# Performance work log

Measured on AMD Instinct MI355X. Metric: run time of the kernel, lower is better.

Reference implementation:

```python
import jax, jax.numpy as jnp
import numpy as np

# MXFP4 e2m1 value lookup (sign bit is the high bit of the nibble)
FP4_LUT = jnp.array([0.0, 0.5, 1.0, 1.5, 2.0, 3.0, 4.0, 6.0,
                     -0.0, -0.5, -1.0, -1.5, -2.0, -3.0, -4.0, -6.0], dtype=jnp.float32)
BLOCK = 32  # mxfp4 scale block size
TOP_K = 2


def dequant_mxfp4(blocks, scales):
    # blocks: [..., K//2] packed uint8 nibbles (low nibble = even elem, high = odd)
    # scales: [..., K//BLOCK] e8m0 biased exponents; scale = 2**(s - 127)
    b = blocks.astype(jnp.int32)
    lo = b & 0xF
    hi = (b >> 4) & 0xF
    nib = jnp.stack([lo, hi], axis=-1).reshape(blocks.shape[:-1] + (blocks.shape[-1] * 2,))
    vals = FP4_LUT[nib]                                   # [..., K]
    s = jnp.exp2(scales.astype(jnp.float32) - 127.0)      # [..., K//BLOCK]
    s = jnp.repeat(s, BLOCK, axis=-1)                     # [..., K]
    return vals * s


def setup_inputs() -> dict:
    key = jax.random.key(0)
    ks = jax.random.split(key, 8)
    E, H, F, B, S = 16, 1024, 2048, 1, 128
    hidden_states = jax.random.normal(ks[0], (B, S, H), dtype=jnp.float32)
    router_w = jax.random.normal(ks[1], (E, H), dtype=jnp.float32) * 0.05
    blocks_gu = jax.random.randint(ks[2], (E, 2 * F, H // 2), 0, 256, dtype=jnp.int32)
    scales_gu = jax.random.randint(ks[3], (E, 2 * F, H // BLOCK), 118, 130, dtype=jnp.int32)
    bias_gu = jax.random.normal(ks[4], (E, 2 * F), dtype=jnp.float32) * 0.02
    blocks_down = jax.random.randint(ks[5], (E, H, F // 2), 0, 256, dtype=jnp.int32)
    scales_down = jax.random.randint(ks[6], (E, H, F // BLOCK), 118, 130, dtype=jnp.int32)
    bias_down = jax.random.normal(ks[7], (E, H), dtype=jnp.float32) * 0.02
    return {"hidden_states": hidden_states, "router_w": router_w,
            "bias_gu": bias_gu, "bias_down": bias_down,
            "blocks_gu": blocks_gu, "scales_gu": scales_gu,
            "blocks_down": blocks_down, "scales_down": scales_down}


def reference(hidden_states, router_w, bias_gu, bias_down,
              blocks_gu, scales_gu, blocks_down, scales_down):
    B, S, H = hidden_states.shape
    flat = hidden_states.reshape(-1, H)                   # [T, H]
    T = flat.shape[0]
    E = router_w.shape[0]

    # --- routing: topk_then_softmax (default softmax_order) ---
    logits = flat @ router_w.T                            # [T, E]
    top_vals, top_idx = jax.lax.top_k(logits, TOP_K)      # [T, K]
    weights = jax.nn.softmax(top_vals, axis=-1).astype(flat.dtype)
    combine = jnp.zeros((T, E), flat.dtype).at[jnp.arange(T)[:, None], top_idx].set(weights)

    # --- mxfp4 dequant of fused expert weights ---
    w_gu = dequant_mxfp4(blocks_gu, scales_gu)            # [E, 2F, H]
    w_down = dequant_mxfp4(blocks_down, scales_down)      # [E, H, F]

    # --- expert MLP (SwiGLU), combined with routing weights ---
    gu = jnp.einsum('th,eoh->eto', flat, w_gu) + bias_gu[:, None, :]   # [E, T, 2F]
    gate, up = jnp.split(gu, 2, axis=-1)
    h = jax.nn.silu(gate) * up                            # [E, T, F]
    y = jnp.einsum('etf,ehf->eth', h, w_down) + bias_down[:, None, :]  # [E, T, H]
    out = jnp.einsum('eth,te->th', y, combine)            # [T, H]
    return out.reshape(B, S, H)
```

## Files before the change

kernel.cpp:

```cpp
#include <hip/hip_runtime.h>
#include <hip/hip_fp16.h>
#include <math.h>

#define NE 16
#define HD 1024
#define FD 2048

typedef _Float16 half8 __attribute__((ext_vector_type(8)));
typedef float f32x4 __attribute__((ext_vector_type(4)));

#define TOPI_OFF 0
#define TOPW_OFF 256
#define CNT_OFF  512
#define PREF_OFF 528
#define SLOT_OFF 544
#define INVT_OFF 800
#define META_OFF 1056
#define TL1_OFF  1060
#define HBUF_OFF 4096
#define Y0_OFF   (HBUF_OFF + 262144)
#define Y1_OFF   (Y0_OFF + 262144)

union XI { int4 v; half8 h; };

__device__ __forceinline__ int fp4h(int nib) {
    int c = nib & 7;
    int v;
    if (c == 0) v = 0;
    else if (c == 1) v = 14 << 10;
    else v = (((c >> 1) + 14) << 10) | ((c & 1) << 9);
    v |= (nib & 8) << 12;
    return v;
}

__device__ __forceinline__ int dec2i(const int* lut, int byte, int sv) {
    int l = lut[byte & 255];
    __half2 p = *reinterpret_cast<const __half2*>(&l);
    __half2 sc = *reinterpret_cast<const __half2*>(&sv);
    __half2 r = __hmul2(p, sc);
    return *reinterpret_cast<int*>(&r);
}

__global__ void routing_kernel(const float* __restrict__ x, const float* __restrict__ rw,
                               int* __restrict__ top_idx, float* __restrict__ top_w) {
    int t = blockIdx.x;
    int tid = threadIdx.x;
    int e = tid >> 4, seg = tid & 15;
    const float* xr = x + t * HD + seg * 64;
    const float* wr = rw + e * HD + seg * 64;
    float p = 0.f;
    #pragma unroll 8
    for (int i = 0; i < 64; ++i) p += xr[i] * wr[i];
    __shared__ float part[16][16];
    __shared__ float logit[16];
    part[e][seg] = p;
    __syncthreads();
    if (tid < 16) {
        float s = 0.f;
        #pragma unroll
        for (int i = 0; i < 16; ++i) s += part[tid][i];
        logit[tid] = s;
    }
    __syncthreads();
    if (tid == 0) {
        int i0 = 0; float v0 = logit[0];
        #pragma unroll
        for (int i = 1; i < 16; ++i) { if (logit[i] > v0) { v0 = logit[i]; i0 = i; } }
        int i1 = -1; float v1 = -1e30f;
        #pragma unroll
        for (int i = 0; i < 16; ++i) { if (i != i0 && logit[i] > v1) { v1 = logit[i]; i1 = i; } }
        float w0 = 1.f / (1.f + expf(v1 - v0));
        float w1 = 1.f / (1.f + expf(v0 - v1));
        top_idx[t * 2]     = i0;  top_w[t * 2]     = w0;
        top_idx[t * 2 + 1] = i1;  top_w[t * 2 + 1] = w1;
    }
}

__global__ void build_kernel(const int* __restrict__ top_idx,
                             int* __restrict__ cnt, int* __restrict__ pref,
                             int* __restrict__ slot, int* __restrict__ invtok,
                             int* __restrict__ meta, int* __restrict__ tl1) {
    __shared__ int scnt[16], spref[16], scur[16];
    int tid = threadIdx.x;
    if (tid < 16) scnt[tid] = 0;
    __syncthreads();
    int e = top_idx[tid];
    atomicAdd(&scnt[e], 1);
    __syncthreads();
    if (tid == 0) {
        int s = 0;
        for (int i = 0; i < 16; ++i) { spref[i] = s; pref[i] = s; cnt[i] = scnt[i]; s += scnt[i]; }
        int m1 = 0;
        for (int i = 0; i < 16; ++i) {
            int ntile1 = (scnt[i] + 15) >> 4;
            for (int m = 0; m < ntile1; ++m) tl1[m1++] = (i << 8) | m;
        }
        meta[0] = m1;
    }
    if (tid < 16) scur[tid] = 0;
    __syncthreads();
    int pos = spref[e] + atomicAdd(&scur[e], 1);
    slot[tid] = pos;
    invtok[pos] = tid >> 1;
}

__global__ __launch_bounds__(256) void gemm1_mfma(
    const float* __restrict__ x, const int* __restrict__ invtok,
    const int* __restrict__ qblk, const int* __restrict__ qscl,
    const float* __restrict__ bias,
    const int* __restrict__ cnt, const int* __restrict__ pref,
    const int* __restrict__ meta, const int* __restrict__ tl1,
    _Float16* __restrict__ hbuf) {
    __shared__ int lut[256];
    __shared__ int4 Asb[2][128];
    __shared__ int4 Bsb[2][512];
    __shared__ float exch[4][64][4];
    int tid = threadIdx.x;
    lut[tid] = fp4h(tid & 15) | (fp4h(tid >> 4) << 16);
    int wave = tid >> 6, lane = tid & 63;
    int bl = lane & 15, kb4 = lane >> 4;
    int rloc = wave * 16 + bl;
    int rs = tid >> 2, kq = tid & 3;
    int tok = tid >> 4, jj = tid & 15;
    int a2idx = (tok * 8 + ((jj >> 1) ^ (tok & 7))) * 2 + (jj & 1);
    int nwork = meta[0] << 6;

    for (int w = blockIdx.x; w < nwork; w += gridDim.x) {
        int tile = tl1[w >> 6];
        int fc = w & 63;
        int e = tile >> 8, mt = tile & 255;
        int n = cnt[e];
        int nt = n - mt * 16; if (nt > 16) nt = 16;
        int base = pref[e];
        int t0 = base + mt * 16;
        int f0 = fc * 32;

        long rowg = (long)e * 4096 + ((rs < 32) ? (f0 + rs) : (2048 + f0 + rs - 32));
        const int4* wrow = (const int4*)(qblk + rowg * 512);
        const int* srow = qscl + rowg * 32;
        int gtok = invtok[t0 + ((tok < nt) ? tok : nt - 1)];
        const int4* arow = (const int4*)x + (long)gtok * 256;

        int4 q0 = wrow[kq * 2];
        int4 q1 = wrow[kq * 2 + 1];
        int sc = srow[kq >> 1];
        int4 av = arow[jj];
        __syncthreads();
        {
            union { int4 v; float f[4]; } uf; uf.v = av;
            union { _Float16 h[4]; int2 p; } o;
            o.h[0] = (_Float16)uf.f[0]; o.h[1] = (_Float16)uf.f[1];
            o.h[2] = (_Float16)uf.f[2]; o.h[3] = (_Float16)uf.f[3];
            ((int2*)Asb[0])[a2idx] = o.p;
            int sv = (sc - 112) << 10; sv |= sv << 16;
            int4 o0, o1;
            o0.x = dec2i(lut, q0.x, sv); o0.y = dec2i(lut, q0.y, sv);
            o0.z = dec2i(lut, q0.z, sv); o0.w = dec2i(lut, q0.w, sv);
            o1.x = dec2i(lut, q1.x, sv); o1.y = dec2i(lut, q1.y, sv);
            o1.z = dec2i(lut, q1.z, sv); o1.w = dec2i(lut, q1.w, sv);
            Bsb[0][rs * 8 + ((kq * 2) ^ (rs & 7))] = o0;
            Bsb[0][rs * 8 + ((kq * 2 + 1) ^ (rs & 7))] = o1;
        }
        __syncthreads();

        f32x4 acc = {0.f, 0.f, 0.f, 0.f};
        for (int kb = 0; kb < 16; ++kb) {
            int cur = kb & 1;
            if (kb < 15) {
                q0 = wrow[(kb + 1) * 8 + kq * 2];
                q1 = wrow[(kb + 1) * 8 + kq * 2 + 1];
                sc = srow[(kb + 1) * 2 + (kq >> 1)];
                av = arow[(kb + 1) * 16 + jj];
            }
            #pragma unroll
            for (int ks = 0; ks < 2; ++ks) {
                int g = ks * 4 + kb4;
                XI a, b;
                a.v = Asb[cur][bl * 8 + (g ^ (bl & 7))];
                b.v = Bsb[cur][rloc * 8 + (g ^ (rloc & 7))];
                acc = __builtin_amdgcn_mfma_f32_16x16x32_f16(a.h, b.h, acc, 0, 0, 0);
            }
            if (kb < 15) {
                int nxt = cur ^ 1;
                union { int4 v; float f[4]; } uf; uf.v = av;
                union { _Float16 h[4]; int2 p; } o;
                o.h[0] = (_Float16)uf.f[0]; o.h[1] = (_Float16)uf.f[1];
                o.h[2] = (_Float16)uf.f[2]; o.h[3] = (_Float16)uf.f[3];
                ((int2*)Asb[nxt])[a2idx] = o.p;
                int sv = (sc - 112) << 10; sv |= sv << 16;
                int4 o0, o1;
                o0.x = dec2i(lut, q0.x, sv); o0.y = dec2i(lut, q0.y, sv);
                o0.z = dec2i(lut, q0.z, sv); o0.w = dec2i(lut, q0.w, sv);
                o1.x = dec2i(lut, q1.x, sv); o1.y = dec2i(lut, q1.y, sv);
                o1.z = dec2i(lut, q1.z, sv); o1.w = dec2i(lut, q1.w, sv);
                Bsb[nxt][rs * 8 + ((kq * 2) ^ (rs & 7))] = o0;
                Bsb[nxt][rs * 8 + ((kq * 2 + 1) ^ (rs & 7))] = o1;
                __syncthreads();
            }
        }
        #pragma unroll
        for (int i = 0; i < 4; ++i) exch[wave][lane][i] = acc[i];
        __syncthreads();
        int fl = tid & 31, wv = fl >> 4, col = fl & 15;
        float bg = bias[(long)e * 4096 + f0 + fl];
        float bu = bias[(long)e * 4096 + 2048 + f0 + fl];
        #pragma unroll
        for (int d = 0; d < 2; ++d) {
            int tk = (tid >> 5) + d * 8;
            int ln = ((tk >> 2) << 4) | col;
            int rg = tk & 3;
            float g = exch[wv][ln][rg] + bg;
            float u = exch[wv + 2][ln][rg] + bu;
            float h = (g / (1.f + expf(-g))) * u;
            if (tk < nt)
                hbuf[(long)(t0 + tk) * FD + f0 + fl] = (_Float16)(h * 0.0625f);
        }
        __syncthreads();
    }
}

__global__ __launch_bounds__(256) void gemm2_mfma(
    const _Float16* __restrict__ hbuf, const int* __restrict__ qblk,
    const int* __restrict__ qscl, const float* __restrict__ bias,
    const int* __restrict__ cnt, const int* __restrict__ pref,
    const int* __restrict__ meta, const int* __restrict__ tl1,
    float* __restrict__ y0p, float* __restrict__ y1p) {
    __shared__ int lut[256];
    __shared__ int4 Asb[2][128];
    __shared__ int4 Bsb[2][512];
    int tid = threadIdx.x;
    lut[tid] = fp4h(tid & 15) | (fp4h(tid >> 4) << 16);
    int wave = tid >> 6, lane = tid & 63;
    int bl = lane & 15, kb4 = lane >> 4;
    int rloc = wave * 16 + bl;
    int rs = tid >> 2, kq = tid & 3;
    int tok = tid >> 3, ga = tid & 7;
    int nwork = meta[0] << 5;

    for (int w = blockIdx.x; w < nwork; w += gridDim.x) {
        int tile = tl1[w >> 5];
        int sub = w & 31;
        int hc = sub & 15, kh = sub >> 4;
        int e = tile >> 8, mt = tile & 255;
        int n = cnt[e];
        int nt = n - mt * 16; if (nt > 16) nt = 16;
        int base = pref[e];
        int t0 = base + mt * 16;
        int h0 = hc * 64;

        long rowg = (long)e * HD + h0 + rs;
        const int4* wrow = (const int4*)(qblk + rowg * 1024) + (kh * 16) * 8;
        const int* srow = qscl + rowg * 64 + kh * 32;
        int tclamp = (tok < nt) ? tok : nt - 1;
        const int4* arow = (const int4*)hbuf + (long)(t0 + tclamp) * 256 + (kh * 16) * 8;

        int4 q0 = wrow[kq * 2];
        int4 q1 = wrow[kq * 2 + 1];
        int sc = srow[kq >> 1];
        int4 av;
        if (tid < 128) av = arow[ga];
        __syncthreads();
        if (tid < 128) Asb[0][tok * 8 + (ga ^ (tok & 7))] = av;
        {
            int sv = (sc - 112) << 10; sv |= sv << 16;
            int4 o0, o1;
            o0.x = dec2i(lut, q0.x, sv); o0.y = dec2i(lut, q0.y, sv);
            o0.z = dec2i(lut, q0.z, sv); o0.w = dec2i(lut, q0.w, sv);
            o1.x = dec2i(lut, q1.x, sv); o1.y = dec2i(lut, q1.y, sv);
            o1.z = dec2i(lut, q1.z, sv); o1.w = dec2i(lut, q1.w, sv);
            Bsb[0][rs * 8 + ((kq * 2) ^ (rs & 7))] = o0;
            Bsb[0][rs * 8 + ((kq * 2 + 1) ^ (rs & 7))] = o1;
        }
        __syncthreads();

        f32x4 acc = {0.f, 0.f, 0.f, 0.f};
        for (int kb = 0; kb < 16; ++kb) {
            int cur = kb & 1;
            if (kb < 15) {
                q0 = wrow[(kb + 1) * 8 + kq * 2];
                q1 = wrow[(kb + 1) * 8 + kq * 2 + 1];
                sc = srow[(kb + 1) * 2 + (kq >> 1)];
                if (tid < 128) av = arow[(kb + 1) * 8 + ga];
            }
            #pragma unroll
            for (int ks = 0; ks < 2; ++ks) {
                int g = ks * 4 + kb4;
                XI a, b;
                a.v = Asb[cur][bl * 8 + (g ^ (bl & 7))];
                b.v = Bsb[cur][rloc * 8 + (g ^ (rloc & 7))];
                acc = __builtin_amdgcn_mfma_f32_16x16x32_f16(a.h, b.h, acc, 0, 0, 0);
            }
            if (kb < 15) {
                int nxt = cur ^ 1;
                if (tid < 128) Asb[nxt][tok * 8 + (ga ^ (tok & 7))] = av;
                int sv = (sc - 112) << 10; sv |= sv << 16;
                int4 o0, o1;
                o0.x = dec2i(lut, q0.x, sv); o0.y = dec2i(lut, q0.y, sv);
                o0.z = dec2i(lut, q0.z, sv); o0.w = dec2i(lut, q0.w, sv);
                o1.x = dec2i(lut, q1.x, sv); o1.y = dec2i(lut, q1.y, sv);
                o1.z = dec2i(lut, q1.z, sv); o1.w = dec2i(lut, q1.w, sv);
                Bsb[nxt][rs * 8 + ((kq * 2) ^ (rs & 7))] = o0;
                Bsb[nxt][rs * 8 + ((kq * 2 + 1) ^ (rs & 7))] = o1;
                __syncthreads();
            }
        }
        int hcol = h0 + wave * 16 + bl;
        float bv = (kh == 0) ? bias[(long)e * HD + hcol] : 0.f;
        float* yp = (kh == 0) ? y0p : y1p;
        #pragma unroll
        for (int r = 0; r < 4; ++r) {
            int row = kb4 * 4 + r;
            if (row < nt)
                yp[(long)(t0 + row) * HD + hcol] = acc[r] * 16.f + bv;
        }
        __syncthreads();
    }
}

__global__ void combine_kernel(const float* __restrict__ y0, const float* __restrict__ y1,
                               const int* __restrict__ slot, const float* __restrict__ topw,
                               float* __restrict__ out) {
    int t = blockIdx.x;
    int i = threadIdx.x;
    int s0 = slot[2 * t], s1 = slot[2 * t + 1];
    float w0 = topw[2 * t], w1 = topw[2 * t + 1];
    float4 a0 = ((const float4*)(y0 + (long)s0 * HD))[i];
    float4 a1 = ((const float4*)(y1 + (long)s0 * HD))[i];
    float4 b0 = ((const float4*)(y0 + (long)s1 * HD))[i];
    float4 b1 = ((const float4*)(y1 + (long)s1 * HD))[i];
    float4 o;
    o.x = w0 * (a0.x + a1.x) + w1 * (b0.x + b1.x);
    o.y = w0 * (a0.y + a1.y) + w1 * (b0.y + b1.y);
    o.z = w0 * (a0.z + a1.z) + w1 * (b0.z + b1.z);
    o.w = w0 * (a0.w + a1.w) + w1 * (b0.w + b1.w);
    ((float4*)(out + (long)t * HD))[i] = o;
}

extern "C" void kernel_launch(void* const* d_in, const int* in_sizes, int n_in,
                              void* d_out, int out_size, void* d_ws, size_t ws_size,
                              hipStream_t stream) {
    const float* x          = (const float*)d_in[0];
    const float* rw         = (const float*)d_in[1];
    const float* bias_gu    = (const float*)d_in[2];
    const float* bias_down  = (const float*)d_in[3];
    const int*   blocks_gu  = (const int*)d_in[4];
    const int*   scales_gu  = (const int*)d_in[5];
    const int*   blocks_down= (const int*)d_in[6];
    const int*   scales_down= (const int*)d_in[7];
    float* out = (float*)d_out;
    int*   wsI = (int*)d_ws;
    float* wsF = (float*)d_ws;
    _Float16* hbuf = (_Float16*)(wsI + HBUF_OFF);
    float*    y0   = wsF + Y0_OFF;
    float*    y1   = wsF + Y1_OFF;

    routing_kernel<<<128, 256, 0, stream>>>(x, rw, wsI + TOPI_OFF, wsF + TOPW_OFF);
    build_kernel<<<1, 256, 0, stream>>>(wsI + TOPI_OFF, wsI + CNT_OFF, wsI + PREF_OFF,
                                        wsI + SLOT_OFF, wsI + INVT_OFF,
                                        wsI + META_OFF, wsI + TL1_OFF);
    gemm1_mfma<<<2048, 256, 0, stream>>>(x, wsI + INVT_OFF, blocks_gu, scales_gu, bias_gu,
                                         wsI + CNT_OFF, wsI + PREF_OFF,
                                         wsI + META_OFF, wsI + TL1_OFF, hbuf);
    gemm2_mfma<<<1024, 256, 0, stream>>>(hbuf, blocks_down, scales_down, bias_down,
                                         wsI + CNT_OFF, wsI + PREF_OFF,
                                         wsI + META_OFF, wsI + TL1_OFF, y0, y1);
    combine_kernel<<<128, 256, 0, stream>>>(y0, y1, wsI + SLOT_OFF, wsF + TOPW_OFF, out);
}
```

Before: 60.74 us.

## Deepen global-load prefetch to two stages and use LDS-only barriers in expert GEMMs

Both expert GEMM kernels now keep two K-blocks of weights and activations in flight in registers, and the K loop is fully unrolled in pairs with fixed LDS buffers. The plain __syncthreads is replaced by an inline-asm barrier that waits only on LDS counters, so outstanding global loads are not drained at each barrier. The goal is to hide global memory latency behind dequant and MFMA work, at the cost of more registers and a hand-written barrier that depends on correct waitcnt semantics. The routing dot product is also vectorised to float4 loads with fma.

```diff
diff --git a/kernel.cpp b/kernel.cpp
--- a/kernel.cpp
+++ b/kernel.cpp
@@ -23,6 +23,8 @@
 
 union XI { int4 v; half8 h; };
 
+#define BARRIER_LDS() asm volatile("s_waitcnt lgkmcnt(0)\ns_barrier" ::: "memory")
+
 __device__ __forceinline__ int fp4h(int nib) {
     int c = nib & 7;
     int v;
@@ -41,16 +43,39 @@
     return *reinterpret_cast<int*>(&r);
 }
 
+__device__ __forceinline__ void stageB(const int* lut, int4* Bbuf, int rs, int kq,
+                                       int4 q0, int4 q1, int sc) {
+    int sv = (sc - 112) << 10; sv |= sv << 16;
+    int4 o0, o1;
+    o0.x = dec2i(lut, q0.x, sv); o0.y = dec2i(lut, q0.y, sv);
+    o0.z = dec2i(lut, q0.z, sv); o0.w = dec2i(lut, q0.w, sv);
+    o1.x = dec2i(lut, q1.x, sv); o1.y = dec2i(lut, q1.y, sv);
+    o1.z = dec2i(lut, q1.z, sv); o1.w = dec2i(lut, q1.w, sv);
+    Bbuf[rs * 8 + ((kq * 2) ^ (rs & 7))] = o0;
+    Bbuf[rs * 8 + ((kq * 2 + 1) ^ (rs & 7))] = o1;
+}
+
+__device__ __forceinline__ void stageA1(int4* Abuf, int a2idx, int4 av) {
+    union { int4 v; float f[4]; } uf; uf.v = av;
+    union { _Float16 h[4]; int2 p; } o;
+    o.h[0] = (_Float16)uf.f[0]; o.h[1] = (_Float16)uf.f[1];
+    o.h[2] = (_Float16)uf.f[2]; o.h[3] = (_Float16)uf.f[3];
+    ((int2*)Abuf)[a2idx] = o.p;
+}
+
 __global__ void routing_kernel(const float* __restrict__ x, const float* __restrict__ rw,
                                int* __restrict__ top_idx, float* __restrict__ top_w) {
     int t = blockIdx.x;
     int tid = threadIdx.x;
     int e = tid >> 4, seg = tid & 15;
-    const float* xr = x + t * HD + seg * 64;
-    const float* wr = rw + e * HD + seg * 64;
+    const float4* xr = (const float4*)(x + t * HD + seg * 64);
+    const float4* wr = (const float4*)(rw + e * HD + seg * 64);
     float p = 0.f;
-    #pragma unroll 8
-    for (int i = 0; i < 64; ++i) p += xr[i] * wr[i];
+    #pragma unroll
+    for (int i = 0; i < 16; ++i) {
+        float4 a = xr[i], b = wr[i];
+        p = fmaf(a.x, b.x, fmaf(a.y, b.y, fmaf(a.z, b.z, fmaf(a.w, b.w, p))));
+    }
     __shared__ float part[16][16];
     __shared__ float logit[16];
     part[e][seg] = p;
@@ -141,62 +166,60 @@
         int gtok = invtok[t0 + ((tok < nt) ? tok : nt - 1)];
         const int4* arow = (const int4*)x + (long)gtok * 256;
 
-        int4 q0 = wrow[kq * 2];
-        int4 q1 = wrow[kq * 2 + 1];
-        int sc = srow[kq >> 1];
-        int4 av = arow[jj];
-        __syncthreads();
-        {
-            union { int4 v; float f[4]; } uf; uf.v = av;
-            union { _Float16 h[4]; int2 p; } o;
-            o.h[0] = (_Float16)uf.f[0]; o.h[1] = (_Float16)uf.f[1];
-            o.h[2] = (_Float16)uf.f[2]; o.h[3] = (_Float16)uf.f[3];
-            ((int2*)Asb[0])[a2idx] = o.p;
-            int sv = (sc - 112) << 10; sv |= sv << 16;
-            int4 o0, o1;
-            o0.x = dec2i(lut, q0.x, sv); o0.y = dec2i(lut, q0.y, sv);
-            o0.z = dec2i(lut, q0.z, sv); o0.w = dec2i(lut, q0.w, sv);
-            o1.x = dec2i(lut, q1.x, sv); o1.y = dec2i(lut, q1.y, sv);
-            o1.z = dec2i(lut, q1.z, sv); o1.w = dec2i(lut, q1.w, sv);
-            Bsb[0][rs * 8 + ((kq * 2) ^ (rs & 7))] = o0;
-            Bsb[0][rs * 8 + ((kq * 2 + 1) ^ (rs & 7))] = o1;
-        }
-        __syncthreads();
+        int4 c0q0 = wrow[kq * 2], c0q1 = wrow[kq * 2 + 1];
+        int  c0sc = srow[kq >> 1];
+        int4 c0av = arow[jj];
+        __syncthreads();
+        stageA1(Asb[0], a2idx, c0av);
+        stageB(lut, Bsb[0], rs, kq, c0q0, c0q1, c0sc);
+        int4 aq0 = wrow[8 + kq * 2], aq1 = wrow[8 + kq * 2 + 1];
+        int  asc = srow[2 + (kq >> 1)];
+        int4 aav = arow[16 + jj];
+        int4 bq0 = wrow[16 + kq * 2], bq1 = wrow[16 + kq * 2 + 1];
+        int  bsc = srow[4 + (kq >> 1)];
+        int4 bav = arow[32 + jj];
+        BARRIER_LDS();
 
         f32x4 acc = {0.f, 0.f, 0.f, 0.f};
-        for (int kb = 0; kb < 16; ++kb) {
-            int cur = kb & 1;
-            if (kb < 15) {
-                q0 = wrow[(kb + 1) * 8 + kq * 2];
-                q1 = wrow[(kb + 1) * 8 + kq * 2 + 1];
-                sc = srow[(kb + 1) * 2 + (kq >> 1)];
-                av = arow[(kb + 1) * 16 + jj];
-            }
+        #pragma unroll
+        for (int p = 0; p < 8; ++p) {
+            int kb = 2 * p;
             #pragma unroll
             for (int ks = 0; ks < 2; ++ks) {
                 int g = ks * 4 + kb4;
                 XI a, b;
-                a.v = Asb[cur][bl * 8 + (g ^ (bl & 7))];
-                b.v = Bsb[cur][rloc * 8 + (g ^ (rloc & 7))];
+                a.v = Asb[0][bl * 8 + (g ^ (bl & 7))];
+                b.v = Bsb[0][rloc * 8 + (g ^ (rloc & 7))];
                 acc = __builtin_amdgcn_mfma_f32_16x16x32_f16(a.h, b.h, acc, 0, 0, 0);
             }
-            if (kb < 15) {
-                int nxt = cur ^ 1;
-                union { int4 v; float f[4]; } uf; uf.v = av;
-                union { _Float16 h[4]; int2 p; } o;
-                o.h[0] = (_Float16)uf.f[0]; o.h[1] = (_Float16)uf.f[1];
-                o.h[2] = (_Float16)uf.f[2]; o.h[3] = (_Float16)uf.f[3];
-                ((int2*)Asb[nxt])[a2idx] = o.p;
-                int sv = (sc - 112) << 10; sv |= sv << 16;
-                int4 o0, o1;
-                o0.x = dec2i(lut, q0.x, sv); o0.y = dec2i(lut, q0.y, sv);
-                o0.z = dec2i(lut, q0.z, sv); o0.w = dec2i(lut, q0.w, sv);
-                o1.x = dec2i(lut, q1.x, sv); o1.y = dec2i(lut, q1.y, sv);
-                o1.z = dec2i(lut, q1.z, sv); o1.w = dec2i(lut, q1.w, sv);
-                Bsb[nxt][rs * 8 + ((kq * 2) ^ (rs & 7))] = o0;
-                Bsb[nxt][rs * 8 + ((kq * 2 + 1) ^ (rs & 7))] = o1;
-                __syncthreads();
-            }
+            stageA1(Asb[1], a2idx, aav);
+            stageB(lut, Bsb[1], rs, kq, aq0, aq1, asc);
+            if (p < 7) {
+                int s = kb + 3;
+                aq0 = wrow[s * 8 + kq * 2]; aq1 = wrow[s * 8 + kq * 2 + 1];
+                asc = srow[s * 2 + (kq >> 1)];
+                aav = arow[s * 16 + jj];
+            }
+            BARRIER_LDS();
+            #pragma unroll
+            for (int ks = 0; ks < 2; ++ks) {
+                int g = ks * 4 + kb4;
+                XI a, b;
+                a.v = Asb[1][bl * 8 + (g ^ (bl & 7))];
+                b.v = Bsb[1][rloc * 8 + (g ^ (rloc & 7))];
+                acc = __builtin_amdgcn_mfma_f32_16x16x32_f16(a.h, b.h, acc, 0, 0, 0);
+            }
+            if (p < 7) {
+                stageA1(Asb[0], a2idx, bav);
+                stageB(lut, Bsb[0], rs, kq, bq0, bq1, bsc);
+                if (p < 6) {
+                    int s = kb + 4;
+                    bq0 = wrow[s * 8 + kq * 2]; bq1 = wrow[s * 8 + kq * 2 + 1];
+                    bsc = srow[s * 2 + (kq >> 1)];
+                    bav = arow[s * 16 + jj];
+                }
+            }
+            BARRIER_LDS();
         }
         #pragma unroll
         for (int i = 0; i < 4; ++i) exch[wave][lane][i] = acc[i];
@@ -235,6 +258,7 @@
     int rloc = wave * 16 + bl;
     int rs = tid >> 2, kq = tid & 3;
     int tok = tid >> 3, ga = tid & 7;
+    int aidx = tok * 8 + (ga ^ (tok & 7));
     int nwork = meta[0] << 5;
 
     for (int w = blockIdx.x; w < nwork; w += gridDim.x) {
@@ -254,55 +278,61 @@
         int tclamp = (tok < nt) ? tok : nt - 1;
         const int4* arow = (const int4*)hbuf + (long)(t0 + tclamp) * 256 + (kh * 16) * 8;
 
-        int4 q0 = wrow[kq * 2];
-        int4 q1 = wrow[kq * 2 + 1];
-        int sc = srow[kq >> 1];
-        int4 av;
-        if (tid < 128) av = arow[ga];
-        __syncthreads();
-        if (tid < 128) Asb[0][tok * 8 + (ga ^ (tok & 7))] = av;
-        {
-            int sv = (sc - 112) << 10; sv |= sv << 16;
-            int4 o0, o1;
-            o0.x = dec2i(lut, q0.x, sv); o0.y = dec2i(lut, q0.y, sv);
-            o0.z = dec2i(lut, q0.z, sv); o0.w = dec2i(lut, q0.w, sv);
-            o1.x = dec2i(lut, q1.x, sv); o1.y = dec2i(lut, q1.y, sv);
-            o1.z = dec2i(lut, q1.z, sv); o1.w = dec2i(lut, q1.w, sv);
-            Bsb[0][rs * 8 + ((kq * 2) ^ (rs & 7))] = o0;
-            Bsb[0][rs * 8 + ((kq * 2 + 1) ^ (rs & 7))] = o1;
-        }
-        __syncthreads();
+        int4 c0q0 = wrow[kq * 2], c0q1 = wrow[kq * 2 + 1];
+        int  c0sc = srow[kq >> 1];
+        int4 c0av;
+        if (tid < 128) c0av = arow[ga];
+        __syncthreads();
+        if (tid < 128) Asb[0][aidx] = c0av;
+        stageB(lut, Bsb[0], rs, kq, c0q0, c0q1, c0sc);
+        int4 aq0 = wrow[8 + kq * 2], aq1 = wrow[8 + kq * 2 + 1];
+        int  asc = srow[2 + (kq >> 1)];
+        int4 aav; if (tid < 128) aav = arow[8 + ga];
+        int4 bq0 = wrow[16 + kq * 2], bq1 = wrow[16 + kq * 2 + 1];
+        int  bsc = srow[4 + (kq >> 1)];
+        int4 bav; if (tid < 128) bav = arow[16 + ga];
+        BARRIER_LDS();
 
         f32x4 acc = {0.f, 0.f, 0.f, 0.f};
-        for (int kb = 0; kb < 16; ++kb) {
-            int cur = kb & 1;
-            if (kb < 15) {
-                q0 = wrow[(kb + 1) * 8 + kq * 2];
-                q1 = wrow[(kb + 1) * 8 + kq * 2 + 1];
-                sc = srow[(kb + 1) * 2 + (kq >> 1)];
-                if (tid < 128) av = arow[(kb + 1) * 8 + ga];
-            }
+        #pragma unroll
+        for (int p = 0; p < 8; ++p) {
+            int kb = 2 * p;
             #pragma unroll
             for (int ks = 0; ks < 2; ++ks) {
                 int g = ks * 4 + kb4;
                 XI a, b;
-                a.v = Asb[cur][bl * 8 + (g ^ (bl & 7))];
-                b.v = Bsb[cur][rloc * 8 + (g ^ (rloc & 7))];
+                a.v = Asb[0][bl * 8 + (g ^ (bl & 7))];
+                b.v = Bsb[0][rloc * 8 + (g ^ (rloc & 7))];
                 acc = __builtin_amdgcn_mfma_f32_16x16x32_f16(a.h, b.h, acc, 0, 0, 0);
             }
-            if (kb < 15) {
-                int nxt = cur ^ 1;
-                if (tid < 128) Asb[nxt][tok * 8 + (ga ^ (tok & 7))] = av;
-                int sv = (sc - 112) << 10; sv |= sv << 16;
-                int4 o0, o1;
-                o0.x = dec2i(lut, q0.x, sv); o0.y = dec2i(lut, q0.y, sv);
-                o0.z = dec2i(lut, q0.z, sv); o0.w = dec2i(lut, q0.w, sv);
-                o1.x = dec2i(lut, q1.x, sv); o1.y = dec2i(lut, q1.y, sv);
-                o1.z = dec2i(lut, q1.z, sv); o1.w = dec2i(lut, q1.w, sv);
-                Bsb[nxt][rs * 8 + ((kq * 2) ^ (rs & 7))] = o0;
-                Bsb[nxt][rs * 8 + ((kq * 2 + 1) ^ (rs & 7))] = o1;
-                __syncthreads();
-            }
+            if (tid < 128) Asb[1][aidx] = aav;
+            stageB(lut, Bsb[1], rs, kq, aq0, aq1, asc);
+            if (p < 7) {
+                int s = kb + 3;
+                aq0 = wrow[s * 8 + kq * 2]; aq1 = wrow[s * 8 + kq * 2 + 1];
+                asc = srow[s * 2 + (kq >> 1)];
+                if (tid < 128) aav = arow[s * 8 + ga];
+            }
+            BARRIER_LDS();
+            #pragma unroll
+            for (int ks = 0; ks < 2; ++ks) {
+                int g = ks * 4 + kb4;
+                XI a, b;
+                a.v = Asb[1][bl * 8 + (g ^ (bl & 7))];
+                b.v = Bsb[1][rloc * 8 + (g ^ (rloc & 7))];
+                acc = __builtin_amdgcn_mfma_f32_16x16x32_f16(a.h, b.h, acc, 0, 0, 0);
+            }
+            if (p < 7) {
+                if (tid < 128) Asb[0][aidx] = bav;
+                stageB(lut, Bsb[0], rs, kq, bq0, bq1, bsc);
+                if (p < 6) {
+                    int s = kb + 4;
+                    bq0 = wrow[s * 8 + kq * 2]; bq1 = wrow[s * 8 + kq * 2 + 1];
+                    bsc = srow[s * 2 + (kq >> 1)];
+                    if (tid < 128) bav = arow[s * 8 + ga];
+                }
+            }
+            BARRIER_LDS();
         }
         int hcol = h0 + wave * 16 + bl;
         float bv = (kh == 0) ? bias[(long)e * HD + hcol] : 0.f;
```

After: 57.67 us (median of 2 runs). 5.1% less time.
